# Kernel optimization log

Hardware: AMD Instinct MI355X
Metric: run time of the kernel (lower is better)

The kernel has to match this reference:

```python
import jax, jax.numpy as jnp
import numpy as np

N_NODES = 50000
N_EDGES = 800000
IN_C, HID_C, OUT_C = 128, 128, 64


def setup_inputs() -> dict:
    key = jax.random.key(0)
    k0, k1, k2, k3 = jax.random.split(key, 4)
    x = jax.random.normal(k0, (N_NODES, IN_C), dtype=jnp.float32)
    edge_index = jax.random.randint(k1, (2, N_EDGES), 0, N_NODES, dtype=jnp.int64)
    edge_weight = jnp.ones((N_EDGES,), dtype=jnp.float32)
    # GCNConv params: lin has no bias; bias added after aggregation
    W1 = jax.random.normal(k2, (IN_C, HID_C), dtype=jnp.float32) * (1.0 / np.sqrt(IN_C))
    b1 = jnp.zeros((HID_C,), dtype=jnp.float32)
    W2 = jax.random.normal(k3, (HID_C, OUT_C), dtype=jnp.float32) * (1.0 / np.sqrt(HID_C))
    b2 = jnp.zeros((OUT_C,), dtype=jnp.float32)
    return {"x": x, "edge_index": edge_index, "edge_weight": edge_weight,
            "W1": W1, "b1": b1, "W2": W2, "b2": b2}


def _gcn_conv(x, W, b, row, col, ew, n):
    # PyG GCNConv (normalize=True, self-loops already appended):
    # h = x W; norm_e = deg[row]^-1/2 * w_e * deg[col]^-1/2; out_i = sum_{e: col=i} norm_e * h[row_e] + b
    h = x @ W
    deg = jax.ops.segment_sum(ew, col, num_segments=n)
    dinv = jnp.where(deg > 0, jax.lax.rsqrt(deg), 0.0)
    norm = dinv[row] * ew * dinv[col]
    out = jax.ops.segment_sum(norm[:, None] * h[row], col, num_segments=n)
    return out + b


def reference(x, edge_index, edge_weight, W1, b1, W2, b2):
    n = x.shape[0]
    loop = jnp.arange(n, dtype=edge_index.dtype)
    row = jnp.concatenate([edge_index[0], loop])
    col = jnp.concatenate([edge_index[1], loop])
    ew = jnp.concatenate([edge_weight, jnp.ones((n,), dtype=edge_weight.dtype)])
    h = jax.nn.softmax(x, axis=1)
    # dropout is identity in eval mode (training=False)
    h = jax.nn.relu(_gcn_conv(h, W1, b1, row, col, ew, n))
    h = _gcn_conv(h, W2, b2, row, col, ew, n)
    return h
```

## Files before the change

kernel.cpp:

```cpp
#include <hip/hip_runtime.h>
#include <math.h>


__global__ void softmax_kernel(const float* __restrict__ x, float* __restrict__ out,
                               int nrows) {
  int gid  = blockIdx.x * blockDim.x + threadIdx.x;
  int row  = gid >> 6;
  int lane = gid & 63;
  if (row >= nrows) return;
  const float2* xr = reinterpret_cast<const float2*>(x + (size_t)row * 128);
  float2 v = xr[lane];
  float m = fmaxf(v.x, v.y);
#pragma unroll
  for (int o = 32; o > 0; o >>= 1) m = fmaxf(m, __shfl_xor(m, o));
  float e0 = expf(v.x - m), e1 = expf(v.y - m);
  float s = e0 + e1;
#pragma unroll
  for (int o = 32; o > 0; o >>= 1) s += __shfl_xor(s, o);
  float inv = 1.0f / s;
  float2 r; r.x = e0 * inv; r.y = e1 * inv;
  reinterpret_cast<float2*>(out + (size_t)row * 128)[lane] = r;
}

__global__ void count_kernel(const int* __restrict__ ei, int* __restrict__ counts, int E) {
  int e = blockIdx.x * blockDim.x + threadIdx.x;
  if (e >= E) return;
  atomicAdd(&counts[ei[(size_t)E + e]], 1);
}

__global__ __launch_bounds__(256) void blocksum_kernel(
    const int* __restrict__ counts, int* __restrict__ blockSum, int n) {
  int i = blockIdx.x * 256 + threadIdx.x;
  int v = (i < n) ? counts[i] : 0;
  int s = v;
#pragma unroll
  for (int o = 32; o > 0; o >>= 1) s += __shfl_down(s, o);
  __shared__ int wsum[4];
  int wid = threadIdx.x >> 6, lane = threadIdx.x & 63;
  if (lane == 0) wsum[wid] = s;
  __syncthreads();
  if (threadIdx.x == 0)
    blockSum[blockIdx.x] = wsum[0] + wsum[1] + wsum[2] + wsum[3];
}

__global__ __launch_bounds__(1024) void blockscan_kernel(
    int* __restrict__ blockSum, int nb, int* __restrict__ offs, int n) {
  __shared__ int arr[1024];
  int t = threadIdx.x;
  int v = (t < nb) ? blockSum[t] : 0;
  arr[t] = v;
  __syncthreads();
  for (int d = 1; d < 1024; d <<= 1) {
    int u = (t >= d) ? arr[t - d] : 0;
    __syncthreads();
    arr[t] += u;
    __syncthreads();
  }
  if (t < nb) blockSum[t] = arr[t] - v;
  if (t == nb - 1) offs[n] = arr[t];
}

__global__ __launch_bounds__(256) void blockwrite_kernel(
    const int* __restrict__ counts, const int* __restrict__ blockSum,
    int* __restrict__ offs, int n) {
  __shared__ int arr[256];
  int t = threadIdx.x;
  int i = blockIdx.x * 256 + t;
  int v = (i < n) ? counts[i] : 0;
  arr[t] = v;
  __syncthreads();
  for (int d = 1; d < 256; d <<= 1) {
    int u = (t >= d) ? arr[t - d] : 0;
    __syncthreads();
    arr[t] += u;
    __syncthreads();
  }
  if (i < n) offs[i] = blockSum[blockIdx.x] + arr[t] - v;
}

__global__ void scatter_kernel(const int* __restrict__ ei, const float* __restrict__ ew,
                               const int* __restrict__ offs, int* __restrict__ cursor,
                               int* __restrict__ csr_src, float* __restrict__ csr_nrm,
                               int E) {
  int e = blockIdx.x * blockDim.x + threadIdx.x;
  if (e >= E) return;
  int r = ei[e];
  int c = ei[(size_t)E + e];
  int pos = offs[c] + atomicAdd(&cursor[c], 1);
  csr_src[pos] = r;
  csr_nrm[pos] = ew[e];
}

__global__ void degseg_kernel(const int* __restrict__ offs,
                              const float* __restrict__ csr_w,
                              float* __restrict__ dinv, int n) {
  int i = blockIdx.x * blockDim.x + threadIdx.x;
  if (i >= n) return;
  int j0 = offs[i], j1 = offs[i + 1];
  float d = 1.0f;
  for (int j = j0; j < j1; ++j) d += csr_w[j];
  dinv[i] = (d > 0.0f) ? (1.0f / sqrtf(d)) : 0.0f;
}

__global__ void scale_kernel(const int* __restrict__ csr_s, float* __restrict__ csr_w,
                             const float* __restrict__ dinv, int E) {
  int j = blockIdx.x * blockDim.x + threadIdx.x;
  if (j >= E) return;
  csr_w[j] *= dinv[csr_s[j]];
}

template <int N>
__global__ __launch_bounds__(256) void gemm_kernel(const float* __restrict__ A,
                                                   const float* __restrict__ W,
                                                   float* __restrict__ C, int M) {
  constexpr int CG  = N / 4;
  constexpr int RG  = 256 / CG;
  constexpr int BM  = RG * 4;
  constexpr int LDA = 132;
  __shared__ float sA[BM][LDA];
  const int t   = threadIdx.x;
  const int tx  = t % CG;
  const int ty  = t / CG;
  const int row0 = blockIdx.x * BM;

  for (int i = t; i < BM * 32; i += 256) {
    int r = i >> 5, c4 = i & 31;
    int gr = row0 + r;
    float4 v = make_float4(0.f, 0.f, 0.f, 0.f);
    if (gr < M) v = reinterpret_cast<const float4*>(A)[(size_t)gr * 32 + c4];
    *reinterpret_cast<float4*>(&sA[r][c4 * 4]) = v;
  }
  __syncthreads();

  float acc[4][4] = {};
#pragma unroll 4
  for (int k = 0; k < 128; ++k) {
    float4 w = reinterpret_cast<const float4*>(W + (size_t)k * N)[tx];
    float a0 = sA[ty * 4 + 0][k];
    float a1 = sA[ty * 4 + 1][k];
    float a2 = sA[ty * 4 + 2][k];
    float a3 = sA[ty * 4 + 3][k];
    acc[0][0] = fmaf(a0, w.x, acc[0][0]); acc[0][1] = fmaf(a0, w.y, acc[0][1]);
    acc[0][2] = fmaf(a0, w.z, acc[0][2]); acc[0][3] = fmaf(a0, w.w, acc[0][3]);
    acc[1][0] = fmaf(a1, w.x, acc[1][0]); acc[1][1] = fmaf(a1, w.y, acc[1][1]);
    acc[1][2] = fmaf(a1, w.z, acc[1][2]); acc[1][3] = fmaf(a1, w.w, acc[1][3]);
    acc[2][0] = fmaf(a2, w.x, acc[2][0]); acc[2][1] = fmaf(a2, w.y, acc[2][1]);
    acc[2][2] = fmaf(a2, w.z, acc[2][2]); acc[2][3] = fmaf(a2, w.w, acc[2][3]);
    acc[3][0] = fmaf(a3, w.x, acc[3][0]); acc[3][1] = fmaf(a3, w.y, acc[3][1]);
    acc[3][2] = fmaf(a3, w.z, acc[3][2]); acc[3][3] = fmaf(a3, w.w, acc[3][3]);
  }

#pragma unroll
  for (int r = 0; r < 4; ++r) {
    int gr = row0 + ty * 4 + r;
    if (gr < M) {
      float4 o = make_float4(acc[r][0], acc[r][1], acc[r][2], acc[r][3]);
      reinterpret_cast<float4*>(C + (size_t)gr * N)[tx] = o;
    }
  }
}

template <bool RELU>
__global__ __launch_bounds__(256) void agg128_kernel(
    const float* __restrict__ H, const float* __restrict__ bias,
    const int* __restrict__ offs, const int* __restrict__ src,
    const float* __restrict__ nrm, const float* __restrict__ dinv,
    float* __restrict__ out, int n) {
  int wave = (blockIdx.x << 2) | (threadIdx.x >> 6);
  int lane = threadIdx.x & 63;
  if (wave >= n) return;
  const int i = wave;
  const float2* H2 = reinterpret_cast<const float2*>(H);
  float2 acc = make_float2(0.f, 0.f);
  int j0 = offs[i], j1 = offs[i + 1];
  int j = j0;
  for (; j + 3 < j1; j += 4) {
    int   s0 = src[j],   s1 = src[j+1], s2 = src[j+2], s3 = src[j+3];
    float w0 = nrm[j],   w1 = nrm[j+1], w2 = nrm[j+2], w3 = nrm[j+3];
    float2 h0 = H2[(size_t)s0 * 64 + lane];
    float2 h1 = H2[(size_t)s1 * 64 + lane];
    float2 h2 = H2[(size_t)s2 * 64 + lane];
    float2 h3 = H2[(size_t)s3 * 64 + lane];
    acc.x = fmaf(w0, h0.x, acc.x); acc.y = fmaf(w0, h0.y, acc.y);
    acc.x = fmaf(w1, h1.x, acc.x); acc.y = fmaf(w1, h1.y, acc.y);
    acc.x = fmaf(w2, h2.x, acc.x); acc.y = fmaf(w2, h2.y, acc.y);
    acc.x = fmaf(w3, h3.x, acc.x); acc.y = fmaf(w3, h3.y, acc.y);
  }
  for (; j < j1; ++j) {
    float w = nrm[j];
    float2 h = H2[(size_t)src[j] * 64 + lane];
    acc.x = fmaf(w, h.x, acc.x); acc.y = fmaf(w, h.y, acc.y);
  }
  float di = dinv[i];
  float2 hs = H2[(size_t)i * 64 + lane];
  float2 b  = reinterpret_cast<const float2*>(bias)[lane];
  float2 o;
  o.x = fmaf(di, acc.x, di * di * hs.x) + b.x;
  o.y = fmaf(di, acc.y, di * di * hs.y) + b.y;
  if (RELU) { o.x = fmaxf(o.x, 0.f); o.y = fmaxf(o.y, 0.f); }
  reinterpret_cast<float2*>(out)[(size_t)i * 64 + lane] = o;
}

template <bool RELU>
__global__ __launch_bounds__(256) void agg64_kernel(
    const float* __restrict__ H, const float* __restrict__ bias,
    const int* __restrict__ offs, const int* __restrict__ src,
    const float* __restrict__ nrm, const float* __restrict__ dinv,
    float* __restrict__ out, int n) {
  int wave = (blockIdx.x << 2) | (threadIdx.x >> 6);
  int lane = threadIdx.x & 63;
  if (wave >= n) return;
  const int i = wave;
  float acc = 0.f;
  int j0 = offs[i], j1 = offs[i + 1];
  int j = j0;
  for (; j + 3 < j1; j += 4) {
    int   s0 = src[j],   s1 = src[j+1], s2 = src[j+2], s3 = src[j+3];
    float w0 = nrm[j],   w1 = nrm[j+1], w2 = nrm[j+2], w3 = nrm[j+3];
    float h0 = H[(size_t)s0 * 64 + lane];
    float h1 = H[(size_t)s1 * 64 + lane];
    float h2 = H[(size_t)s2 * 64 + lane];
    float h3 = H[(size_t)s3 * 64 + lane];
    acc = fmaf(w0, h0, acc);
    acc = fmaf(w1, h1, acc);
    acc = fmaf(w2, h2, acc);
    acc = fmaf(w3, h3, acc);
  }
  for (; j < j1; ++j) acc = fmaf(nrm[j], H[(size_t)src[j] * 64 + lane], acc);
  float di = dinv[i];
  float hs = H[(size_t)i * 64 + lane];
  float o  = fmaf(di, acc, di * di * hs) + bias[lane];
  if (RELU) o = fmaxf(o, 0.f);
  out[(size_t)i * 64 + lane] = o;
}

static inline size_t ws_align(size_t x) { return (x + 255) & ~(size_t)255; }

extern "C" void kernel_launch(void* const* d_in, const int* in_sizes, int n_in,
                              void* d_out, int out_size, void* d_ws, size_t ws_size,
                              hipStream_t stream) {
  const float* x  = (const float*)d_in[0];
  const int*   ei = (const int*)d_in[1];
  const float* ew = (const float*)d_in[2];
  const float* W1 = (const float*)d_in[3];
  const float* b1 = (const float*)d_in[4];
  const float* W2 = (const float*)d_in[5];
  const float* b2 = (const float*)d_in[6];
  float*       out = (float*)d_out;

  const int n = in_sizes[0] / 128;
  const int E = in_sizes[2];
  const int nb = (n + 255) / 256;

  char* ws = (char*)d_ws;
  size_t off = 0;
  auto alloc = [&](size_t bytes) -> char* {
    char* p = ws + off;
    off = ws_align(off + bytes);
    return p;
  };
  float* bufA   = (float*)alloc((size_t)n * 128 * sizeof(float));
  float* bufB   = (float*)alloc((size_t)n * 128 * sizeof(float));
  char*  zbase  = ws + off;
  int*   counts = (int*)  alloc((size_t)n * sizeof(int));
  int*   cursor = (int*)  alloc((size_t)n * sizeof(int));
  size_t zbytes = (size_t)((ws + off) - zbase);
  float* dinv   = (float*)alloc((size_t)n * sizeof(float));
  int*   offs   = (int*)  alloc((size_t)(n + 1) * sizeof(int));
  int*   bsum   = (int*)  alloc((size_t)1024 * sizeof(int));
  int*   csr_s  = (int*)  alloc((size_t)E * sizeof(int));
  float* csr_w  = (float*)alloc((size_t)E * sizeof(float));
  (void)ws_size; (void)n_in; (void)out_size;

  hipMemsetAsync(zbase, 0, zbytes, stream);

  count_kernel<<<(E + 255) / 256, 256, 0, stream>>>(ei, counts, E);
  blocksum_kernel<<<nb, 256, 0, stream>>>(counts, bsum, n);
  blockscan_kernel<<<1, 1024, 0, stream>>>(bsum, nb, offs, n);
  blockwrite_kernel<<<nb, 256, 0, stream>>>(counts, bsum, offs, n);
  scatter_kernel<<<(E + 255) / 256, 256, 0, stream>>>(ei, ew, offs, cursor,
                                                      csr_s, csr_w, E);
  degseg_kernel<<<(n + 255) / 256, 256, 0, stream>>>(offs, csr_w, dinv, n);
  scale_kernel<<<(E + 255) / 256, 256, 0, stream>>>(csr_s, csr_w, dinv, E);

  softmax_kernel<<<((size_t)n * 64 + 255) / 256, 256, 0, stream>>>(x, bufA, n);
  gemm_kernel<128><<<(n + 31) / 32, 256, 0, stream>>>(bufA, W1, bufB, n);
  agg128_kernel<true><<<(n + 3) / 4, 256, 0, stream>>>(bufB, b1, offs, csr_s,
                                                       csr_w, dinv, bufA, n);
  gemm_kernel<64><<<(n + 63) / 64, 256, 0, stream>>>(bufA, W2, bufB, n);
  agg64_kernel<false><<<(n + 3) / 4, 256, 0, stream>>>(bufB, b2, offs, csr_s,
                                                       csr_w, dinv, out, n);
}
```

Baseline: 365.8 us.

## Record atomic slot at count time and pack CSR source/weight into int2

The count kernel now stores the atomicAdd return value per edge, so the scatter kernel places edges without a second atomic pass and the cursor array and its memset are dropped. The CSR source index and weight are interleaved into a single int2 array, so the aggregation, degree and scale kernels fetch both with one 8-byte load. The cost is an extra E-sized slot array that is written and then read back.

```diff
diff --git a/kernel.cpp b/kernel.cpp
--- a/kernel.cpp
+++ b/kernel.cpp
@@ -22,10 +22,11 @@
   reinterpret_cast<float2*>(out + (size_t)row * 128)[lane] = r;
 }
 
-__global__ void count_kernel(const int* __restrict__ ei, int* __restrict__ counts, int E) {
+__global__ void count_kernel(const int* __restrict__ ei, int* __restrict__ counts,
+                             int* __restrict__ slot, int E) {
   int e = blockIdx.x * blockDim.x + threadIdx.x;
   if (e >= E) return;
-  atomicAdd(&counts[ei[(size_t)E + e]], 1);
+  slot[e] = atomicAdd(&counts[ei[(size_t)E + e]], 1);
 }
 
 __global__ __launch_bounds__(256) void blocksum_kernel(
@@ -79,34 +80,34 @@
 }
 
 __global__ void scatter_kernel(const int* __restrict__ ei, const float* __restrict__ ew,
-                               const int* __restrict__ offs, int* __restrict__ cursor,
-                               int* __restrict__ csr_src, float* __restrict__ csr_nrm,
-                               int E) {
+                               const int* __restrict__ offs, const int* __restrict__ slot,
+                               int2* __restrict__ pairs, int E) {
   int e = blockIdx.x * blockDim.x + threadIdx.x;
   if (e >= E) return;
   int r = ei[e];
   int c = ei[(size_t)E + e];
-  int pos = offs[c] + atomicAdd(&cursor[c], 1);
-  csr_src[pos] = r;
-  csr_nrm[pos] = ew[e];
+  int pos = offs[c] + slot[e];
+  pairs[pos] = make_int2(r, __float_as_int(ew[e]));
 }
 
 __global__ void degseg_kernel(const int* __restrict__ offs,
-                              const float* __restrict__ csr_w,
+                              const int2* __restrict__ pairs,
                               float* __restrict__ dinv, int n) {
   int i = blockIdx.x * blockDim.x + threadIdx.x;
   if (i >= n) return;
   int j0 = offs[i], j1 = offs[i + 1];
   float d = 1.0f;
-  for (int j = j0; j < j1; ++j) d += csr_w[j];
+  for (int j = j0; j < j1; ++j) d += __int_as_float(pairs[j].y);
   dinv[i] = (d > 0.0f) ? (1.0f / sqrtf(d)) : 0.0f;
 }
 
-__global__ void scale_kernel(const int* __restrict__ csr_s, float* __restrict__ csr_w,
+__global__ void scale_kernel(int2* __restrict__ pairs,
                              const float* __restrict__ dinv, int E) {
   int j = blockIdx.x * blockDim.x + threadIdx.x;
   if (j >= E) return;
-  csr_w[j] *= dinv[csr_s[j]];
+  int2 p = pairs[j];
+  p.y = __float_as_int(__int_as_float(p.y) * dinv[p.x]);
+  pairs[j] = p;
 }
 
 template <int N>
@@ -163,9 +164,8 @@
 template <bool RELU>
 __global__ __launch_bounds__(256) void agg128_kernel(
     const float* __restrict__ H, const float* __restrict__ bias,
-    const int* __restrict__ offs, const int* __restrict__ src,
-    const float* __restrict__ nrm, const float* __restrict__ dinv,
-    float* __restrict__ out, int n) {
+    const int* __restrict__ offs, const int2* __restrict__ pairs,
+    const float* __restrict__ dinv, float* __restrict__ out, int n) {
   int wave = (blockIdx.x << 2) | (threadIdx.x >> 6);
   int lane = threadIdx.x & 63;
   if (wave >= n) return;
@@ -175,20 +175,22 @@
   int j0 = offs[i], j1 = offs[i + 1];
   int j = j0;
   for (; j + 3 < j1; j += 4) {
-    int   s0 = src[j],   s1 = src[j+1], s2 = src[j+2], s3 = src[j+3];
-    float w0 = nrm[j],   w1 = nrm[j+1], w2 = nrm[j+2], w3 = nrm[j+3];
-    float2 h0 = H2[(size_t)s0 * 64 + lane];
-    float2 h1 = H2[(size_t)s1 * 64 + lane];
-    float2 h2 = H2[(size_t)s2 * 64 + lane];
-    float2 h3 = H2[(size_t)s3 * 64 + lane];
+    int2 p0 = pairs[j],   p1 = pairs[j+1], p2 = pairs[j+2], p3 = pairs[j+3];
+    float2 h0 = H2[(size_t)p0.x * 64 + lane];
+    float2 h1 = H2[(size_t)p1.x * 64 + lane];
+    float2 h2 = H2[(size_t)p2.x * 64 + lane];
+    float2 h3 = H2[(size_t)p3.x * 64 + lane];
+    float w0 = __int_as_float(p0.y), w1 = __int_as_float(p1.y);
+    float w2 = __int_as_float(p2.y), w3 = __int_as_float(p3.y);
     acc.x = fmaf(w0, h0.x, acc.x); acc.y = fmaf(w0, h0.y, acc.y);
     acc.x = fmaf(w1, h1.x, acc.x); acc.y = fmaf(w1, h1.y, acc.y);
     acc.x = fmaf(w2, h2.x, acc.x); acc.y = fmaf(w2, h2.y, acc.y);
     acc.x = fmaf(w3, h3.x, acc.x); acc.y = fmaf(w3, h3.y, acc.y);
   }
   for (; j < j1; ++j) {
-    float w = nrm[j];
-    float2 h = H2[(size_t)src[j] * 64 + lane];
+    int2 p = pairs[j];
+    float w = __int_as_float(p.y);
+    float2 h = H2[(size_t)p.x * 64 + lane];
     acc.x = fmaf(w, h.x, acc.x); acc.y = fmaf(w, h.y, acc.y);
   }
   float di = dinv[i];
@@ -204,9 +206,8 @@
 template <bool RELU>
 __global__ __launch_bounds__(256) void agg64_kernel(
     const float* __restrict__ H, const float* __restrict__ bias,
-    const int* __restrict__ offs, const int* __restrict__ src,
-    const float* __restrict__ nrm, const float* __restrict__ dinv,
-    float* __restrict__ out, int n) {
+    const int* __restrict__ offs, const int2* __restrict__ pairs,
+    const float* __restrict__ dinv, float* __restrict__ out, int n) {
   int wave = (blockIdx.x << 2) | (threadIdx.x >> 6);
   int lane = threadIdx.x & 63;
   if (wave >= n) return;
@@ -215,18 +216,20 @@
   int j0 = offs[i], j1 = offs[i + 1];
   int j = j0;
   for (; j + 3 < j1; j += 4) {
-    int   s0 = src[j],   s1 = src[j+1], s2 = src[j+2], s3 = src[j+3];
-    float w0 = nrm[j],   w1 = nrm[j+1], w2 = nrm[j+2], w3 = nrm[j+3];
-    float h0 = H[(size_t)s0 * 64 + lane];
-    float h1 = H[(size_t)s1 * 64 + lane];
-    float h2 = H[(size_t)s2 * 64 + lane];
-    float h3 = H[(size_t)s3 * 64 + lane];
-    acc = fmaf(w0, h0, acc);
-    acc = fmaf(w1, h1, acc);
-    acc = fmaf(w2, h2, acc);
-    acc = fmaf(w3, h3, acc);
-  }
-  for (; j < j1; ++j) acc = fmaf(nrm[j], H[(size_t)src[j] * 64 + lane], acc);
+    int2 p0 = pairs[j],   p1 = pairs[j+1], p2 = pairs[j+2], p3 = pairs[j+3];
+    float h0 = H[(size_t)p0.x * 64 + lane];
+    float h1 = H[(size_t)p1.x * 64 + lane];
+    float h2 = H[(size_t)p2.x * 64 + lane];
+    float h3 = H[(size_t)p3.x * 64 + lane];
+    acc = fmaf(__int_as_float(p0.y), h0, acc);
+    acc = fmaf(__int_as_float(p1.y), h1, acc);
+    acc = fmaf(__int_as_float(p2.y), h2, acc);
+    acc = fmaf(__int_as_float(p3.y), h3, acc);
+  }
+  for (; j < j1; ++j) {
+    int2 p = pairs[j];
+    acc = fmaf(__int_as_float(p.y), H[(size_t)p.x * 64 + lane], acc);
+  }
   float di = dinv[i];
   float hs = H[(size_t)i * 64 + lane];
   float o  = fmaf(di, acc, di * di * hs) + bias[lane];
@@ -263,31 +266,29 @@
   float* bufB   = (float*)alloc((size_t)n * 128 * sizeof(float));
   char*  zbase  = ws + off;
   int*   counts = (int*)  alloc((size_t)n * sizeof(int));
-  int*   cursor = (int*)  alloc((size_t)n * sizeof(int));
   size_t zbytes = (size_t)((ws + off) - zbase);
   float* dinv   = (float*)alloc((size_t)n * sizeof(float));
   int*   offs   = (int*)  alloc((size_t)(n + 1) * sizeof(int));
   int*   bsum   = (int*)  alloc((size_t)1024 * sizeof(int));
-  int*   csr_s  = (int*)  alloc((size_t)E * sizeof(int));
-  float* csr_w  = (float*)alloc((size_t)E * sizeof(float));
+  int*   slot   = (int*)  alloc((size_t)E * sizeof(int));
+  int2*  pairs  = (int2*) alloc((size_t)E * sizeof(int2));
   (void)ws_size; (void)n_in; (void)out_size;
 
   hipMemsetAsync(zbase, 0, zbytes, stream);
 
-  count_kernel<<<(E + 255) / 256, 256, 0, stream>>>(ei, counts, E);
+  count_kernel<<<(E + 255) / 256, 256, 0, stream>>>(ei, counts, slot, E);
   blocksum_kernel<<<nb, 256, 0, stream>>>(counts, bsum, n);
   blockscan_kernel<<<1, 1024, 0, stream>>>(bsum, nb, offs, n);
   blockwrite_kernel<<<nb, 256, 0, stream>>>(counts, bsum, offs, n);
-  scatter_kernel<<<(E + 255) / 256, 256, 0, stream>>>(ei, ew, offs, cursor,
-                                                      csr_s, csr_w, E);
-  degseg_kernel<<<(n + 255) / 256, 256, 0, stream>>>(offs, csr_w, dinv, n);
-  scale_kernel<<<(E + 255) / 256, 256, 0, stream>>>(csr_s, csr_w, dinv, E);
+  scatter_kernel<<<(E + 255) / 256, 256, 0, stream>>>(ei, ew, offs, slot, pairs, E);
+  degseg_kernel<<<(n + 255) / 256, 256, 0, stream>>>(offs, pairs, dinv, n);
+  scale_kernel<<<(E + 255) / 256, 256, 0, stream>>>(pairs, dinv, E);
 
   softmax_kernel<<<((size_t)n * 64 + 255) / 256, 256, 0, stream>>>(x, bufA, n);
   gemm_kernel<128><<<(n + 31) / 32, 256, 0, stream>>>(bufA, W1, bufB, n);
-  agg128_kernel<true><<<(n + 3) / 4, 256, 0, stream>>>(bufB, b1, offs, csr_s,
-                                                       csr_w, dinv, bufA, n);
+  agg128_kernel<true><<<(n + 3) / 4, 256, 0, stream>>>(bufB, b1, offs, pairs,
+                                                       dinv, bufA, n);
   gemm_kernel<64><<<(n + 63) / 64, 256, 0, stream>>>(bufA, W2, bufB, n);
-  agg64_kernel<false><<<(n + 3) / 4, 256, 0, stream>>>(bufB, b2, offs, csr_s,
-                                                       csr_w, dinv, out, n);
-}
+  agg64_kernel<false><<<(n + 3) / 4, 256, 0, stream>>>(bufB, b2, offs, pairs,
+                                                       dinv, out, n);
+}
```

Measured after the change: 322.9 us. 1.13x faster.
